# Kernel tuning notes

Measured on AMD Instinct MI355X. Metric: run time of the kernel, lower is better.

## Reference

```python
import jax, jax.numpy as jnp
import numpy as np

N_HEAD, D_MODEL, D_K, D_V = 16, 1024, 64, 64
B, S = 2, 2048
NEG = -1e10
LN_EPS = 1e-5

def setup_inputs() -> dict:
    key = jax.random.key(0)
    ks = jax.random.split(key, 10)
    std = 1.0 / np.sqrt(D_MODEL)
    return {
        "q": jax.random.normal(ks[0], (B, S, D_MODEL), jnp.float32),
        "k": jax.random.normal(ks[1], (B, S, D_MODEL), jnp.float32),
        "v": jax.random.normal(ks[2], (B, S, D_MODEL), jnp.float32),
        "mask": jnp.ones((B, 1, 1, S), jnp.int32),
        "Wq": jax.random.normal(ks[3], (D_MODEL, N_HEAD * D_K), jnp.float32) * std,
        "Wk": jax.random.normal(ks[4], (D_MODEL, N_HEAD * D_K), jnp.float32) * std,
        "Wv": jax.random.normal(ks[5], (D_MODEL, N_HEAD * D_V), jnp.float32) * std,
        "Wo": jax.random.normal(ks[6], (N_HEAD * D_V, D_MODEL), jnp.float32) * std,
        "bo": jnp.zeros((D_MODEL,), jnp.float32),
        "gamma": jnp.ones((D_MODEL,), jnp.float32),
        "beta": jnp.zeros((D_MODEL,), jnp.float32),
    }

def reference(q, k, v, mask, Wq, Wk, Wv, Wo, bo, gamma, beta):
    b, s, _ = q.shape
    scale = np.sqrt(D_MODEL)  # NOTE: original scales by sqrt(d_model), not sqrt(d_k)
    # project and split heads: [B,S,H,Dk] -> [B,H,S,Dk]
    qs = (q @ Wq).reshape(b, s, N_HEAD, D_K).transpose(0, 2, 1, 3)
    kk = (k @ Wk).reshape(b, -1, N_HEAD, D_K).transpose(0, 2, 1, 3)
    vs = (v @ Wv).reshape(b, -1, N_HEAD, D_V).transpose(0, 2, 1, 3)
    attn = jnp.einsum("bhqd,bhkd->bhqk", qs, kk) / scale
    attn = jnp.where(mask == 0, NEG, attn)
    attn = jax.nn.softmax(attn, axis=-1)  # dropout is identity in eval mode
    out = jnp.einsum("bhqk,bhkd->bhqd", attn, vs)
    out = out.transpose(0, 2, 1, 3).reshape(b, s, N_HEAD * D_V)
    out = out @ Wo + bo
    x = out + q
    mu = jnp.mean(x, axis=-1, keepdims=True)
    var = jnp.var(x, axis=-1, keepdims=True)
    out = (x - mu) * jax.lax.rsqrt(var + LN_EPS) * gamma + beta
    return out, attn
```

## Files before the change

kernel.cpp:

```cpp
#include <hip/hip_runtime.h>
#include <stdint.h>
#include <stddef.h>

#define NHEAD 16
#define DMODEL 1024
#define SS 2048
#define BB 2

typedef __attribute__((ext_vector_type(8))) short bf16x8;
typedef __attribute__((ext_vector_type(4))) float f32x4;
typedef __attribute__((ext_vector_type(4))) float floatv4;
typedef __attribute__((ext_vector_type(4))) unsigned short ushortv4;
typedef __attribute__((ext_vector_type(8))) unsigned short ushortv8;

#define MFMA16(A, B, C) __builtin_amdgcn_mfma_f32_16x16x32_bf16(A, B, C, 0, 0, 0)

__device__ __forceinline__ unsigned short f2bf(float f) {
    union { float f; unsigned u; } x;
    x.f = f;
    unsigned r = x.u + 0x7FFFu + ((x.u >> 16) & 1u);
    return (unsigned short)(r >> 16);
}

__device__ __forceinline__ unsigned short f2bf_trunc(float f) {
    union { float f; unsigned u; } x;
    x.f = f;
    return (unsigned short)(x.u >> 16);
}

__device__ __forceinline__ float bf2f(unsigned short u) {
    union { unsigned u; float f; } x;
    x.u = ((unsigned)u) << 16;
    return x.f;
}

__global__ __launch_bounds__(256) void cvt3(const float* __restrict__ q,
                                            const float* __restrict__ k,
                                            const float* __restrict__ v,
                                            unsigned short* __restrict__ qb,
                                            unsigned short* __restrict__ kb,
                                            unsigned short* __restrict__ vb, int n4) {
    int i = blockIdx.x * 256 + threadIdx.x;
    if (i >= n4) return;
    const float* src = blockIdx.y == 0 ? q : (blockIdx.y == 1 ? k : v);
    unsigned short* dst = blockIdx.y == 0 ? qb : (blockIdx.y == 1 ? kb : vb);
    floatv4 x = ((const floatv4*)src)[i];
    ushortv4 o;
    o.x = f2bf(x.x); o.y = f2bf(x.y); o.z = f2bf(x.z); o.w = f2bf(x.w);
    ((ushortv4*)dst)[i] = o;
}

__global__ __launch_bounds__(256) void wtrans4(
    const float* __restrict__ W0, const float* __restrict__ W1,
    const float* __restrict__ W2, const float* __restrict__ W3,
    unsigned short* __restrict__ T0, unsigned short* __restrict__ T1,
    unsigned short* __restrict__ T2, unsigned short* __restrict__ T3) {
    int sel = blockIdx.z;
    const float* W = sel == 0 ? W0 : (sel == 1 ? W1 : (sel == 2 ? W2 : W3));
    unsigned short* Wt = sel == 0 ? T0 : (sel == 1 ? T1 : (sel == 2 ? T2 : T3));
    float scl = (sel == 0) ? 0.03125f : 1.0f;
    __shared__ float tile[32][33];
    int tx = threadIdx.x & 31, ty = threadIdx.x >> 5;
    int nb = blockIdx.x * 32, kb = blockIdx.y * 32;
#pragma unroll
    for (int i = 0; i < 4; i++)
        tile[ty + i * 8][tx] = W[(size_t)(kb + ty + i * 8) * DMODEL + nb + tx];
    __syncthreads();
#pragma unroll
    for (int i = 0; i < 4; i++)
        Wt[(size_t)(nb + ty + i * 8) * DMODEL + kb + tx] = f2bf(tile[tx][ty + i * 8] * scl);
}

__device__ __forceinline__ void stage_tile_sw(const unsigned short* __restrict__ src, int ld,
                                              unsigned short* lds) {
    int t = threadIdx.x;
#pragma unroll
    for (int i = 0; i < 4; i++) {
        int pos = i * 256 + t;
        int row = pos >> 3;
        int g = pos & 7;
        int kcol = (g ^ (row & 7)) * 8;
        __builtin_amdgcn_global_load_lds(
            (__attribute__((address_space(1))) void*)(src + row * ld + kcol),
            (__attribute__((address_space(3))) void*)(lds + pos * 8), 16, 0, 0);
    }
}

__device__ __forceinline__ bf16x8 frag_ld(const unsigned short* lds, int row, int koff) {
    int idx = row * 64 + (koff ^ ((row & 7) << 3));
    return *(const bf16x8*)(lds + idx);
}

__device__ __forceinline__ void gemm_core(const unsigned short* __restrict__ A,
                                          const unsigned short* __restrict__ Bt,
                                          int mbase, int nbase,
                                          unsigned short* As, unsigned short* Bs,
                                          f32x4 acc[4][4]) {
    int tid = threadIdx.x;
    int w = tid >> 6, lane = tid & 63, lg = lane >> 4, li = lane & 15;
    int wm = w >> 1, wn = w & 1;
#pragma unroll
    for (int mi = 0; mi < 4; mi++)
#pragma unroll
        for (int ni = 0; ni < 4; ni++) acc[mi][ni] = f32x4{0.f, 0.f, 0.f, 0.f};

    for (int ks = 0; ks < DMODEL / 64; ks++) {
        __syncthreads();
        stage_tile_sw(A + (size_t)mbase * DMODEL + ks * 64, DMODEL, As);
        stage_tile_sw(Bt + (size_t)nbase * DMODEL + ks * 64, DMODEL, Bs);
        __syncthreads();
        bf16x8 af[2][4], bfr[2][4];
#pragma unroll
        for (int kc = 0; kc < 2; kc++) {
#pragma unroll
            for (int mi = 0; mi < 4; mi++)
                af[kc][mi] = frag_ld(As, wm * 64 + mi * 16 + li, kc * 32 + lg * 8);
#pragma unroll
            for (int ni = 0; ni < 4; ni++)
                bfr[kc][ni] = frag_ld(Bs, wn * 64 + ni * 16 + li, kc * 32 + lg * 8);
        }
#pragma unroll
        for (int kc = 0; kc < 2; kc++)
#pragma unroll
            for (int mi = 0; mi < 4; mi++)
#pragma unroll
                for (int ni = 0; ni < 4; ni++)
                    acc[mi][ni] = MFMA16(af[kc][mi], bfr[kc][ni], acc[mi][ni]);
    }
}

#define CS_STRIDE 136

__global__ __launch_bounds__(256) void gemm_qkv(
    const unsigned short* __restrict__ qb, const unsigned short* __restrict__ kbuf,
    const unsigned short* __restrict__ vb,
    const unsigned short* __restrict__ Wqt, const unsigned short* __restrict__ Wkt,
    const unsigned short* __restrict__ Wvt,
    unsigned short* __restrict__ Qp, unsigned short* __restrict__ Kp,
    unsigned short* __restrict__ Vt) {
    __shared__ unsigned short LDSbuf[128 * CS_STRIDE];
    unsigned short* As = LDSbuf;
    unsigned short* Bs = LDSbuf + 128 * 64;
    unsigned short* Cs = LDSbuf;

    int bid = blockIdx.y * 24 + blockIdx.x;
    int nl = (bid & 7) * 96 + (bid >> 3);
    int nt = nl % 24;
    int mbase = (nl / 24) * 128;
    int seg = nt >> 3;
    int nbase = (nt & 7) * 128;
    const unsigned short* A = seg == 0 ? qb : (seg == 1 ? kbuf : vb);
    const unsigned short* Bt = seg == 0 ? Wqt : (seg == 1 ? Wkt : Wvt);

    f32x4 acc[4][4];
    gemm_core(A, Bt, mbase, nbase, As, Bs, acc);

    int tid = threadIdx.x, w = tid >> 6, lane = tid & 63, lg = lane >> 4, li = lane & 15;
    int wm = w >> 1, wn = w & 1;

    __syncthreads();
    if (seg == 2) {
#pragma unroll
        for (int mi = 0; mi < 4; mi++)
#pragma unroll
            for (int ni = 0; ni < 4; ni++) {
                int nloc = wn * 64 + ni * 16 + li;
                int mloc = wm * 64 + mi * 16 + lg * 4;
#pragma unroll
                for (int r = 0; r < 4; r++)
                    Cs[nloc * CS_STRIDE + mloc + r] = f2bf(acc[mi][ni][r]);
            }
        __syncthreads();
#pragma unroll
        for (int i = 0; i < 8; i++) {
            int g = i * 256 + tid;
            int nloc = g >> 4, mo = (g & 15) * 8;
            int ng = nbase + nloc, h = ng >> 6, d = ng & 63;
            int m0 = mbase + mo, b = m0 >> 11, s0 = m0 & 2047;
            *(ushortv8*)(Vt + (((size_t)((b * NHEAD + h) * 64 + d)) << 11) + s0) =
                *(const ushortv8*)(Cs + nloc * CS_STRIDE + mo);
        }
    } else {
        unsigned short* Out = seg == 0 ? Qp : Kp;
#pragma unroll
        for (int mi = 0; mi < 4; mi++)
#pragma unroll
            for (int ni = 0; ni < 4; ni++) {
                int nloc = wn * 64 + ni * 16 + li;
                int mloc = wm * 64 + mi * 16 + lg * 4;
#pragma unroll
                for (int r = 0; r < 4; r++)
                    Cs[(mloc + r) * CS_STRIDE + nloc] = f2bf(acc[mi][ni][r]);
            }
        __syncthreads();
#pragma unroll
        for (int i = 0; i < 8; i++) {
            int g = i * 256 + tid;
            int row = g >> 4, on = (g & 15) * 8;
            int ng = nbase + on, h = ng >> 6, d = ng & 63;
            int m0 = mbase + row, b = m0 >> 11, s0 = m0 & 2047;
            *(ushortv8*)(Out + ((size_t)((b * NHEAD + h) * SS + s0)) * 64 + d) =
                *(const ushortv8*)(Cs + row * CS_STRIDE + on);
        }
    }
}

__global__ __launch_bounds__(256) void gemm_out(
    const unsigned short* __restrict__ Ob, const unsigned short* __restrict__ Wot,
    unsigned short* __restrict__ Yb) {
    __shared__ unsigned short LDSbuf[128 * CS_STRIDE];
    unsigned short* As = LDSbuf;
    unsigned short* Bs = LDSbuf + 128 * 64;
    unsigned short* Cs = LDSbuf;

    int bid = blockIdx.y * 8 + blockIdx.x;
    int nl = (bid & 7) * 32 + (bid >> 3);
    int nbase = (nl % 8) * 128;
    int mbase = (nl / 8) * 128;

    f32x4 acc[4][4];
    gemm_core(Ob, Wot, mbase, nbase, As, Bs, acc);

    int tid = threadIdx.x, w = tid >> 6, lane = tid & 63, lg = lane >> 4, li = lane & 15;
    int wm = w >> 1, wn = w & 1;

    __syncthreads();
#pragma unroll
    for (int mi = 0; mi < 4; mi++)
#pragma unroll
        for (int ni = 0; ni < 4; ni++) {
            int nloc = wn * 64 + ni * 16 + li;
            int mloc = wm * 64 + mi * 16 + lg * 4;
#pragma unroll
            for (int r = 0; r < 4; r++)
                Cs[(mloc + r) * CS_STRIDE + nloc] = f2bf(acc[mi][ni][r]);
        }
    __syncthreads();
#pragma unroll
    for (int i = 0; i < 8; i++) {
        int g = i * 256 + tid;
        int row = g >> 4, on = (g & 15) * 8;
        *(ushortv8*)(Yb + (size_t)(mbase + row) * DMODEL + nbase + on) =
            *(const ushortv8*)(Cs + row * CS_STRIDE + on);
    }
}

__device__ __forceinline__ void stage_kv(const unsigned short* __restrict__ Kb,
                                         const unsigned short* __restrict__ Vtb, int s0,
                                         unsigned short* kl, unsigned short* vl, int tid) {
#pragma unroll
    for (int i = 0; i < 2; i++) {
        int pos = i * 256 + tid;
        int row = pos >> 3, g = pos & 7;
        int col = (g ^ (row & 7)) * 8;
        __builtin_amdgcn_global_load_lds(
            (__attribute__((address_space(1))) void*)(Kb + (size_t)(s0 + row) * 64 + col),
            (__attribute__((address_space(3))) void*)(kl + pos * 8), 16, 0, 0);
    }
#pragma unroll
    for (int i = 0; i < 2; i++) {
        int pos = i * 256 + tid;
        int row = pos >> 3, g = pos & 7;
        int col = (g ^ (row & 7)) * 8;
        __builtin_amdgcn_global_load_lds(
            (__attribute__((address_space(1))) void*)(Vtb + (size_t)row * SS + s0 + col),
            (__attribute__((address_space(3))) void*)(vl + pos * 8), 16, 0, 0);
    }
}

__global__ __launch_bounds__(256, 2) void attn_fused(
    const unsigned short* __restrict__ Qp, const unsigned short* __restrict__ Kp,
    const unsigned short* __restrict__ Vt, const int* __restrict__ mask,
    float* __restrict__ attn_out, unsigned short* __restrict__ Ob) {
    __shared__ unsigned short Ks[2][64 * 64];
    __shared__ unsigned short Vs[2][64 * 64];
    __shared__ unsigned short Pl[4][32 * 64];
    __shared__ float Ml[SS];

    int blk = blockIdx.x;
    int xslot = blk & 7, rest = blk >> 3;
    int qt = rest & 15, bg = rest >> 4;
    int bh = bg * 8 + xslot, b = bh >> 4;
    int q0 = qt * 128;
    int tid = threadIdx.x, w = tid >> 6, lane = tid & 63, lg = lane >> 4, li = lane & 15;
    const unsigned short* Qb = Qp + (size_t)bh * SS * 64;
    const unsigned short* Kb = Kp + (size_t)bh * SS * 64;
    const unsigned short* Vtb = Vt + (size_t)bh * 64 * SS;
    const int* mb = mask + b * SS;
    int qw = q0 + w * 32;
    int sw = (li & 7) << 3;

    stage_kv(Kb, Vtb, 0, &Ks[0][0], &Vs[0][0], tid);

#pragma unroll
    for (int i = 0; i < SS / 256; i++) {
        int idx = i * 256 + tid;
        Ml[idx] = mb[idx] ? 0.f : -1e10f;
    }

    bf16x8 qa[2][2];
#pragma unroll
    for (int fq = 0; fq < 2; fq++) {
        int q = qw + fq * 16 + li;
        qa[fq][0] = *(const bf16x8*)(Qb + (size_t)q * 64 + lg * 8);
        qa[fq][1] = *(const bf16x8*)(Qb + (size_t)q * 64 + 32 + lg * 8);
    }

    f32x4 oacc[2][4];
#pragma unroll
    for (int fq = 0; fq < 2; fq++)
#pragma unroll
        for (int gd = 0; gd < 4; gd++) oacc[fq][gd] = f32x4{0.f, 0.f, 0.f, 0.f};
    float lsA[2] = {0.f, 0.f}, lsB[2] = {0.f, 0.f};
    unsigned short* Pw = &Pl[w][0];

    asm volatile("s_waitcnt vmcnt(0) lgkmcnt(0)" ::: "memory");
    __builtin_amdgcn_s_barrier();

#pragma unroll 1
    for (int t = 0; t < 32; t++) {
        int k0 = t * 64;
        if (t + 1 < 32)
            stage_kv(Kb, Vtb, k0 + 64, &Ks[(t + 1) & 1][0], &Vs[(t + 1) & 1][0], tid);
        __builtin_amdgcn_sched_barrier(0);
        const unsigned short* Kc = &Ks[t & 1][0];
        const unsigned short* Vc = &Vs[t & 1][0];
#pragma unroll
        for (int fk = 0; fk < 4; fk++) {
            int row = fk * 16 + li;
            bf16x8 kf0 = *(const bf16x8*)(Kc + row * 64 + ((lg * 8) ^ sw));
            bf16x8 kf1 = *(const bf16x8*)(Kc + row * 64 + ((32 + lg * 8) ^ sw));
            floatv4 mk = *(const floatv4*)(Ml + k0 + fk * 16 + lg * 4);
#pragma unroll
            for (int fq = 0; fq < 2; fq++) {
                f32x4 sc = f32x4{0.f, 0.f, 0.f, 0.f};
                sc = MFMA16(kf0, qa[fq][0], sc);
                sc = MFMA16(kf1, qa[fq][1], sc);
                floatv4 pv;
#pragma unroll
                for (int r = 0; r < 4; r++)
                    pv[r] = __expf(fminf(sc[r] + mk[r], 80.f));
                lsA[fq] += pv[0] + pv[1];
                lsB[fq] += pv[2] + pv[3];
                ushortv4 pk;
#pragma unroll
                for (int r = 0; r < 4; r++) pk[r] = f2bf_trunc(pv[r]);
                *(ushortv4*)(Pw + (fq * 16 + li) * 64 + ((fk * 16 + lg * 4) ^ sw)) = pk;
            }
        }
#pragma unroll
        for (int kc = 0; kc < 2; kc++) {
            bf16x8 vf[4];
#pragma unroll
            for (int gd = 0; gd < 4; gd++) {
                int vrow = gd * 16 + li;
                vf[gd] = *(const bf16x8*)(Vc + vrow * 64 + ((kc * 32 + lg * 8) ^ sw));
            }
#pragma unroll
            for (int fq = 0; fq < 2; fq++) {
                bf16x8 pa = *(const bf16x8*)(Pw + (fq * 16 + li) * 64 +
                                             ((kc * 32 + lg * 8) ^ sw));
#pragma unroll
                for (int gd = 0; gd < 4; gd++)
                    oacc[fq][gd] = MFMA16(pa, vf[gd], oacc[fq][gd]);
            }
        }
        asm volatile("s_waitcnt vmcnt(0)" ::: "memory");
        __builtin_amdgcn_s_barrier();
    }

    float linvv[2];
    float* LinvW = (float*)Pw;
#pragma unroll
    for (int fq = 0; fq < 2; fq++) {
        float lsum = lsA[fq] + lsB[fq];
        lsum += __shfl_xor(lsum, 16);
        lsum += __shfl_xor(lsum, 32);
        linvv[fq] = 1.0f / lsum;
        if (lg == 0) LinvW[fq * 16 + li] = linvv[fq];
    }
    int h = bh & 15;
#pragma unroll
    for (int fq = 0; fq < 2; fq++)
#pragma unroll
        for (int gd = 0; gd < 4; gd++)
#pragma unroll
            for (int r = 0; r < 4; r++) {
                int srow = qw + fq * 16 + lg * 4 + r;
                float o = oacc[fq][gd][r] * LinvW[fq * 16 + lg * 4 + r];
                Ob[(size_t)(b * SS + srow) * DMODEL + h * 64 + gd * 16 + li] = f2bf(o);
            }

    float* ar0 = attn_out + ((size_t)bh * SS + qw + li) * SS + lg * 4;
    float* ar1 = ar0 + (size_t)16 * SS;
#pragma unroll 1
    for (int kt = 0; kt < 16; kt++) {
        int k0 = kt * 128;
#pragma unroll
        for (int fk = 0; fk < 8; fk++) {
            const unsigned short* kp = Kb + (size_t)(k0 + fk * 16 + li) * 64;
            bf16x8 kf0 = *(const bf16x8*)(kp + lg * 8);
            bf16x8 kf1 = *(const bf16x8*)(kp + 32 + lg * 8);
            floatv4 mk = *(const floatv4*)(Ml + k0 + fk * 16 + lg * 4);
#pragma unroll
            for (int fq = 0; fq < 2; fq++) {
                f32x4 sc = f32x4{0.f, 0.f, 0.f, 0.f};
                sc = MFMA16(kf0, qa[fq][0], sc);
                sc = MFMA16(kf1, qa[fq][1], sc);
                floatv4 pv;
#pragma unroll
                for (int r = 0; r < 4; r++)
                    pv[r] = __expf(fminf(sc[r] + mk[r], 80.f)) * linvv[fq];
                *(floatv4*)((fq == 0 ? ar0 : ar1) + k0 + fk * 16) = pv;
            }
        }
    }
}

__global__ __launch_bounds__(256) void ln_kernel(const unsigned short* __restrict__ Yb,
                                                 const float* __restrict__ qres,
                                                 const float* __restrict__ bo,
                                                 const float* __restrict__ gamma,
                                                 const float* __restrict__ beta,
                                                 float* __restrict__ out) {
    int row = blockIdx.x;
    int t = threadIdx.x;
    ushortv4 yv = ((const ushortv4*)(Yb + (size_t)row * DMODEL))[t];
    floatv4 qv = ((const floatv4*)(qres + (size_t)row * DMODEL))[t];
    floatv4 bv = ((const floatv4*)bo)[t];
    floatv4 v;
    v.x = bf2f(yv.x) + bv.x + qv.x;
    v.y = bf2f(yv.y) + bv.y + qv.y;
    v.z = bf2f(yv.z) + bv.z + qv.z;
    v.w = bf2f(yv.w) + bv.w + qv.w;
    float s1 = v.x + v.y + v.z + v.w;
    float s2 = v.x * v.x + v.y * v.y + v.z * v.z + v.w * v.w;
#pragma unroll
    for (int m = 1; m < 64; m <<= 1) { s1 += __shfl_xor(s1, m); s2 += __shfl_xor(s2, m); }
    __shared__ float red[8];
    int w = t >> 6, lane = t & 63;
    if (lane == 0) { red[w] = s1; red[4 + w] = s2; }
    __syncthreads();
    s1 = red[0] + red[1] + red[2] + red[3];
    s2 = red[4] + red[5] + red[6] + red[7];
    float mu = s1 * (1.0f / DMODEL);
    float var = s2 * (1.0f / DMODEL) - mu * mu;
    float rstd = rsqrtf(var + 1e-5f);
    floatv4 g = ((const floatv4*)gamma)[t];
    floatv4 bb = ((const floatv4*)beta)[t];
    floatv4 o;
    o.x = (v.x - mu) * rstd * g.x + bb.x;
    o.y = (v.y - mu) * rstd * g.y + bb.y;
    o.z = (v.z - mu) * rstd * g.z + bb.z;
    o.w = (v.w - mu) * rstd * g.w + bb.w;
    ((floatv4*)(out + (size_t)row * DMODEL))[t] = o;
}

extern "C" void kernel_launch(void* const* d_in, const int* in_sizes, int n_in,
                              void* d_out, int out_size, void* d_ws, size_t ws_size,
                              hipStream_t stream) {
    const float* q = (const float*)d_in[0];
    const float* k = (const float*)d_in[1];
    const float* v = (const float*)d_in[2];
    const int* mask = (const int*)d_in[3];
    const float* Wq = (const float*)d_in[4];
    const float* Wk = (const float*)d_in[5];
    const float* Wv = (const float*)d_in[6];
    const float* Wo = (const float*)d_in[7];
    const float* bo = (const float*)d_in[8];
    const float* gamma = (const float*)d_in[9];
    const float* beta = (const float*)d_in[10];

    float* out = (float*)d_out;
    float* attn = out + (size_t)BB * SS * DMODEL;

    const size_t NTOK = (size_t)BB * SS;
    unsigned short* qb = (unsigned short*)d_ws;
    unsigned short* kb = qb + NTOK * DMODEL;
    unsigned short* vb = kb + NTOK * DMODEL;
    unsigned short* Wqt = vb + NTOK * DMODEL;
    unsigned short* Wkt = Wqt + (size_t)DMODEL * DMODEL;
    unsigned short* Wvt = Wkt + (size_t)DMODEL * DMODEL;
    unsigned short* Wot = Wvt + (size_t)DMODEL * DMODEL;
    unsigned short* Qp = Wot + (size_t)DMODEL * DMODEL;
    unsigned short* Kp = Qp + NTOK * DMODEL;
    unsigned short* Vt = Kp + NTOK * DMODEL;
    unsigned short* Ob = Vt + NTOK * DMODEL;
    unsigned short* Yb = qb;

    const int n4 = (int)(NTOK * DMODEL / 4);
    cvt3<<<dim3(n4 / 256, 3), 256, 0, stream>>>(q, k, v, qb, kb, vb, n4);
    wtrans4<<<dim3(32, 32, 4), 256, 0, stream>>>(Wq, Wk, Wv, Wo, Wqt, Wkt, Wvt, Wot);

    gemm_qkv<<<dim3(24, 32), 256, 0, stream>>>(qb, kb, vb, Wqt, Wkt, Wvt, Qp, Kp, Vt);

    attn_fused<<<512, 256, 0, stream>>>(Qp, Kp, Vt, mask, attn, Ob);

    gemm_out<<<dim3(8, 32), 256, 0, stream>>>(Ob, Wot, Yb);

    ln_kernel<<<(int)NTOK, 256, 0, stream>>>(Yb, q, bo, gamma, beta, out);
}
```

Measured before the change: 301.5 us.

## Split fused attention into output kernel and separate attention-probability writer kernel

Splits the fused attention kernel in two. The first kernel computes the output and stores per-row inverse softmax sums to global memory. It keeps the mask in LDS as bf16 to shrink shared memory and raises the occupancy hint to 3 blocks per CU. A second kernel with 4x more blocks recomputes QK^T over key slices and writes the large fp32 attention matrix, spreading that write-bound phase across more parallel blocks. The cost is an extra launch and recomputing scores a second time.

```diff
diff --git a/kernel.cpp b/kernel.cpp
--- a/kernel.cpp
+++ b/kernel.cpp
@@ -268,14 +268,14 @@
     }
 }
 
-__global__ __launch_bounds__(256, 2) void attn_fused(
+__global__ __launch_bounds__(256, 3) void attn_o(
     const unsigned short* __restrict__ Qp, const unsigned short* __restrict__ Kp,
     const unsigned short* __restrict__ Vt, const int* __restrict__ mask,
-    float* __restrict__ attn_out, unsigned short* __restrict__ Ob) {
+    float* __restrict__ linvG, unsigned short* __restrict__ Ob) {
     __shared__ unsigned short Ks[2][64 * 64];
     __shared__ unsigned short Vs[2][64 * 64];
     __shared__ unsigned short Pl[4][32 * 64];
-    __shared__ float Ml[SS];
+    __shared__ unsigned short Mlb[SS];
 
     int blk = blockIdx.x;
     int xslot = blk & 7, rest = blk >> 3;
@@ -295,7 +295,7 @@
 #pragma unroll
     for (int i = 0; i < SS / 256; i++) {
         int idx = i * 256 + tid;
-        Ml[idx] = mb[idx] ? 0.f : -1e10f;
+        Mlb[idx] = mb[idx] ? (unsigned short)0 : f2bf_trunc(-1e10f);
     }
 
     bf16x8 qa[2][2];
@@ -330,7 +330,10 @@
             int row = fk * 16 + li;
             bf16x8 kf0 = *(const bf16x8*)(Kc + row * 64 + ((lg * 8) ^ sw));
             bf16x8 kf1 = *(const bf16x8*)(Kc + row * 64 + ((32 + lg * 8) ^ sw));
-            floatv4 mk = *(const floatv4*)(Ml + k0 + fk * 16 + lg * 4);
+            ushortv4 mku = *(const ushortv4*)(Mlb + k0 + fk * 16 + lg * 4);
+            float mkf[4];
+#pragma unroll
+            for (int r = 0; r < 4; r++) mkf[r] = bf2f(mku[r]);
 #pragma unroll
             for (int fq = 0; fq < 2; fq++) {
                 f32x4 sc = f32x4{0.f, 0.f, 0.f, 0.f};
@@ -339,7 +342,7 @@
                 floatv4 pv;
 #pragma unroll
                 for (int r = 0; r < 4; r++)
-                    pv[r] = __expf(fminf(sc[r] + mk[r], 80.f));
+                    pv[r] = __expf(fminf(sc[r] + mkf[r], 80.f));
                 lsA[fq] += pv[0] + pv[1];
                 lsB[fq] += pv[2] + pv[3];
                 ushortv4 pk;
@@ -377,7 +380,10 @@
         lsum += __shfl_xor(lsum, 16);
         lsum += __shfl_xor(lsum, 32);
         linvv[fq] = 1.0f / lsum;
-        if (lg == 0) LinvW[fq * 16 + li] = linvv[fq];
+        if (lg == 0) {
+            LinvW[fq * 16 + li] = linvv[fq];
+            linvG[(size_t)bh * SS + qw + fq * 16 + li] = linvv[fq];
+        }
     }
     int h = bh & 15;
 #pragma unroll
@@ -390,15 +396,52 @@
                 float o = oacc[fq][gd][r] * LinvW[fq * 16 + lg * 4 + r];
                 Ob[(size_t)(b * SS + srow) * DMODEL + h * 64 + gd * 16 + li] = f2bf(o);
             }
-
-    float* ar0 = attn_out + ((size_t)bh * SS + qw + li) * SS + lg * 4;
+}
+
+__global__ __launch_bounds__(256) void attn_p(
+    const unsigned short* __restrict__ Qp, const unsigned short* __restrict__ Kp,
+    const int* __restrict__ mask, const float* __restrict__ linvG,
+    float* __restrict__ attn_out) {
+    __shared__ float Ml[512];
+    int blk = blockIdx.x;
+    int xslot = blk & 7, rest = blk >> 3;
+    int qt = rest & 15; rest >>= 4;
+    int ksl = rest & 3; rest >>= 2;
+    int bg = rest;
+    int bh = bg * 8 + xslot, b = bh >> 4;
+    int q0 = qt * 128;
+    int kbase = ksl * 512;
+    int tid = threadIdx.x, w = tid >> 6, lane = tid & 63, lg = lane >> 4, li = lane & 15;
+    const unsigned short* Qb = Qp + (size_t)bh * SS * 64;
+    const unsigned short* Kb = Kp + (size_t)bh * SS * 64;
+    const int* mb = mask + b * SS + kbase;
+    int qw = q0 + w * 32;
+
+#pragma unroll
+    for (int i = 0; i < 2; i++) {
+        int idx = i * 256 + tid;
+        Ml[idx] = mb[idx] ? 0.f : -1e10f;
+    }
+    __syncthreads();
+
+    bf16x8 qa[2][2];
+    float lv[2];
+#pragma unroll
+    for (int fq = 0; fq < 2; fq++) {
+        int q = qw + fq * 16 + li;
+        qa[fq][0] = *(const bf16x8*)(Qb + (size_t)q * 64 + lg * 8);
+        qa[fq][1] = *(const bf16x8*)(Qb + (size_t)q * 64 + 32 + lg * 8);
+        lv[fq] = linvG[(size_t)bh * SS + q];
+    }
+    float* ar0 = attn_out + ((size_t)bh * SS + qw + li) * SS + kbase + lg * 4;
     float* ar1 = ar0 + (size_t)16 * SS;
+
 #pragma unroll 1
-    for (int kt = 0; kt < 16; kt++) {
+    for (int kt = 0; kt < 4; kt++) {
         int k0 = kt * 128;
 #pragma unroll
         for (int fk = 0; fk < 8; fk++) {
-            const unsigned short* kp = Kb + (size_t)(k0 + fk * 16 + li) * 64;
+            const unsigned short* kp = Kb + (size_t)(kbase + k0 + fk * 16 + li) * 64;
             bf16x8 kf0 = *(const bf16x8*)(kp + lg * 8);
             bf16x8 kf1 = *(const bf16x8*)(kp + 32 + lg * 8);
             floatv4 mk = *(const floatv4*)(Ml + k0 + fk * 16 + lg * 4);
@@ -410,7 +453,7 @@
                 floatv4 pv;
 #pragma unroll
                 for (int r = 0; r < 4; r++)
-                    pv[r] = __expf(fminf(sc[r] + mk[r], 80.f)) * linvv[fq];
+                    pv[r] = __expf(fminf(sc[r] + mk[r], 80.f)) * lv[fq];
                 *(floatv4*)((fq == 0 ? ar0 : ar1) + k0 + fk * 16) = pv;
             }
         }
@@ -486,6 +529,7 @@
     unsigned short* Kp = Qp + NTOK * DMODEL;
     unsigned short* Vt = Kp + NTOK * DMODEL;
     unsigned short* Ob = Vt + NTOK * DMODEL;
+    float* linvG = (float*)(Ob + NTOK * DMODEL);
     unsigned short* Yb = qb;
 
     const int n4 = (int)(NTOK * DMODEL / 4);
@@ -494,7 +538,8 @@
 
     gemm_qkv<<<dim3(24, 32), 256, 0, stream>>>(qb, kb, vb, Wqt, Wkt, Wvt, Qp, Kp, Vt);
 
-    attn_fused<<<512, 256, 0, stream>>>(Qp, Kp, Vt, mask, attn, Ob);
+    attn_o<<<512, 256, 0, stream>>>(Qp, Kp, Vt, mask, linvG, Ob);
+    attn_p<<<2048, 256, 0, stream>>>(Qp, Kp, mask, linvG, attn);
 
     gemm_out<<<dim3(8, 32), 256, 0, stream>>>(Ob, Wot, Yb);
 
```

Measured after the change: 349.9 us. 1.16x slower.

## Stage attention-probability writes through LDS for coalesced rows; merge prep kernels

Applied to the files above, without the earlier changes.

The attention-probability output pass now writes each 64-column tile into a per-wave swizzled LDS buffer, reusing the freed K/V/P shared memory, then reads it back so each row segment goes to global memory as contiguous 256-byte stores. Before, each lane wrote scattered 16-byte chunks across rows. This targets the large fp32 attn write, which dominates memory traffic. Separately, the bf16 conversion and weight-transpose kernels are merged into one launch to save a kernel launch. The cost is extra LDS traffic and a barrier.

```diff
diff --git a/kernel.cpp b/kernel.cpp
--- a/kernel.cpp
+++ b/kernel.cpp
@@ -34,41 +34,43 @@
     return x.f;
 }
 
-__global__ __launch_bounds__(256) void cvt3(const float* __restrict__ q,
-                                            const float* __restrict__ k,
-                                            const float* __restrict__ v,
-                                            unsigned short* __restrict__ qb,
-                                            unsigned short* __restrict__ kb,
-                                            unsigned short* __restrict__ vb, int n4) {
-    int i = blockIdx.x * 256 + threadIdx.x;
-    if (i >= n4) return;
-    const float* src = blockIdx.y == 0 ? q : (blockIdx.y == 1 ? k : v);
-    unsigned short* dst = blockIdx.y == 0 ? qb : (blockIdx.y == 1 ? kb : vb);
-    floatv4 x = ((const floatv4*)src)[i];
-    ushortv4 o;
-    o.x = f2bf(x.x); o.y = f2bf(x.y); o.z = f2bf(x.z); o.w = f2bf(x.w);
-    ((ushortv4*)dst)[i] = o;
-}
-
-__global__ __launch_bounds__(256) void wtrans4(
+__global__ __launch_bounds__(256) void prep(
+    const float* __restrict__ q, const float* __restrict__ k, const float* __restrict__ v,
+    unsigned short* __restrict__ qb, unsigned short* __restrict__ kb,
+    unsigned short* __restrict__ vb,
     const float* __restrict__ W0, const float* __restrict__ W1,
     const float* __restrict__ W2, const float* __restrict__ W3,
     unsigned short* __restrict__ T0, unsigned short* __restrict__ T1,
     unsigned short* __restrict__ T2, unsigned short* __restrict__ T3) {
-    int sel = blockIdx.z;
-    const float* W = sel == 0 ? W0 : (sel == 1 ? W1 : (sel == 2 ? W2 : W3));
-    unsigned short* Wt = sel == 0 ? T0 : (sel == 1 ? T1 : (sel == 2 ? T2 : T3));
-    float scl = (sel == 0) ? 0.03125f : 1.0f;
     __shared__ float tile[32][33];
-    int tx = threadIdx.x & 31, ty = threadIdx.x >> 5;
-    int nb = blockIdx.x * 32, kb = blockIdx.y * 32;
-#pragma unroll
-    for (int i = 0; i < 4; i++)
-        tile[ty + i * 8][tx] = W[(size_t)(kb + ty + i * 8) * DMODEL + nb + tx];
-    __syncthreads();
-#pragma unroll
-    for (int i = 0; i < 4; i++)
-        Wt[(size_t)(nb + ty + i * 8) * DMODEL + kb + tx] = f2bf(tile[tx][ty + i * 8] * scl);
+    int blk = blockIdx.x;
+    if (blk < 12288) {
+        int which = blk >> 12;
+        int i = (blk & 4095) * 256 + threadIdx.x;
+        const float* src = which == 0 ? q : (which == 1 ? k : v);
+        unsigned short* dst = which == 0 ? qb : (which == 1 ? kb : vb);
+        floatv4 x = ((const floatv4*)src)[i];
+        ushortv4 o;
+        o.x = f2bf(x.x); o.y = f2bf(x.y); o.z = f2bf(x.z); o.w = f2bf(x.w);
+        ((ushortv4*)dst)[i] = o;
+    } else {
+        int t = blk - 12288;
+        int sel = t >> 10;
+        int rest = t & 1023;
+        const float* W = sel == 0 ? W0 : (sel == 1 ? W1 : (sel == 2 ? W2 : W3));
+        unsigned short* Wt = sel == 0 ? T0 : (sel == 1 ? T1 : (sel == 2 ? T2 : T3));
+        float scl = (sel == 0) ? 0.03125f : 1.0f;
+        int tx = threadIdx.x & 31, ty = threadIdx.x >> 5;
+        int nb = (rest & 31) * 32, kb2 = (rest >> 5) * 32;
+#pragma unroll
+        for (int i = 0; i < 4; i++)
+            tile[ty + i * 8][tx] = W[(size_t)(kb2 + ty + i * 8) * DMODEL + nb + tx];
+        __syncthreads();
+#pragma unroll
+        for (int i = 0; i < 4; i++)
+            Wt[(size_t)(nb + ty + i * 8) * DMODEL + kb2 + tx] =
+                f2bf(tile[tx][ty + i * 8] * scl);
+    }
 }
 
 __device__ __forceinline__ void stage_tile_sw(const unsigned short* __restrict__ src, int ld,
@@ -272,10 +274,11 @@
     const unsigned short* __restrict__ Qp, const unsigned short* __restrict__ Kp,
     const unsigned short* __restrict__ Vt, const int* __restrict__ mask,
     float* __restrict__ attn_out, unsigned short* __restrict__ Ob) {
-    __shared__ unsigned short Ks[2][64 * 64];
-    __shared__ unsigned short Vs[2][64 * 64];
-    __shared__ unsigned short Pl[4][32 * 64];
-    __shared__ float Ml[SS];
+    __shared__ __align__(16) unsigned short SH[28672];
+    unsigned short* KsB = SH;
+    unsigned short* VsB = SH + 8192;
+    unsigned short* PlB = SH + 16384;
+    float* Ml = (float*)(SH + 24576);
 
     int blk = blockIdx.x;
     int xslot = blk & 7, rest = blk >> 3;
@@ -290,7 +293,7 @@
     int qw = q0 + w * 32;
     int sw = (li & 7) << 3;
 
-    stage_kv(Kb, Vtb, 0, &Ks[0][0], &Vs[0][0], tid);
+    stage_kv(Kb, Vtb, 0, KsB, VsB, tid);
 
 #pragma unroll
     for (int i = 0; i < SS / 256; i++) {
@@ -312,7 +315,7 @@
 #pragma unroll
         for (int gd = 0; gd < 4; gd++) oacc[fq][gd] = f32x4{0.f, 0.f, 0.f, 0.f};
     float lsA[2] = {0.f, 0.f}, lsB[2] = {0.f, 0.f};
-    unsigned short* Pw = &Pl[w][0];
+    unsigned short* Pw = PlB + w * (32 * 64);
 
     asm volatile("s_waitcnt vmcnt(0) lgkmcnt(0)" ::: "memory");
     __builtin_amdgcn_s_barrier();
@@ -321,10 +324,11 @@
     for (int t = 0; t < 32; t++) {
         int k0 = t * 64;
         if (t + 1 < 32)
-            stage_kv(Kb, Vtb, k0 + 64, &Ks[(t + 1) & 1][0], &Vs[(t + 1) & 1][0], tid);
+            stage_kv(Kb, Vtb, k0 + 64, KsB + ((t + 1) & 1) * 4096,
+                     VsB + ((t + 1) & 1) * 4096, tid);
         __builtin_amdgcn_sched_barrier(0);
-        const unsigned short* Kc = &Ks[t & 1][0];
-        const unsigned short* Vc = &Vs[t & 1][0];
+        const unsigned short* Kc = KsB + (t & 1) * 4096;
+        const unsigned short* Vc = VsB + (t & 1) * 4096;
 #pragma unroll
         for (int fk = 0; fk < 4; fk++) {
             int row = fk * 16 + li;
@@ -391,13 +395,15 @@
                 Ob[(size_t)(b * SS + srow) * DMODEL + h * 64 + gd * 16 + li] = f2bf(o);
             }
 
-    float* ar0 = attn_out + ((size_t)bh * SS + qw + li) * SS + lg * 4;
-    float* ar1 = ar0 + (size_t)16 * SS;
+    __builtin_amdgcn_s_barrier();
+    float* Pt = (float*)SH + w * 2048;
+    int rgrp = lane >> 4;
+
 #pragma unroll 1
-    for (int kt = 0; kt < 16; kt++) {
-        int k0 = kt * 128;
-#pragma unroll
-        for (int fk = 0; fk < 8; fk++) {
+    for (int t = 0; t < 32; t++) {
+        int k0 = t * 64;
+#pragma unroll
+        for (int fk = 0; fk < 4; fk++) {
             const unsigned short* kp = Kb + (size_t)(k0 + fk * 16 + li) * 64;
             bf16x8 kf0 = *(const bf16x8*)(kp + lg * 8);
             bf16x8 kf1 = *(const bf16x8*)(kp + 32 + lg * 8);
@@ -411,8 +417,16 @@
 #pragma unroll
                 for (int r = 0; r < 4; r++)
                     pv[r] = __expf(fminf(sc[r] + mk[r], 80.f)) * linvv[fq];
-                *(floatv4*)((fq == 0 ? ar0 : ar1) + k0 + fk * 16) = pv;
-            }
+                int prow = fq * 16 + li;
+                *(floatv4*)(Pt + prow * 64 + ((fk * 16 + lg * 4) ^ ((prow & 7) << 3))) = pv;
+            }
+        }
+#pragma unroll
+        for (int g = 0; g < 8; g++) {
+            int row = g * 4 + rgrp;
+            int colb = li * 4;
+            floatv4 vv = *(const floatv4*)(Pt + row * 64 + (colb ^ ((row & 7) << 3)));
+            *(floatv4*)(attn_out + ((size_t)bh * SS + qw + row) * SS + k0 + colb) = vv;
         }
     }
 }
@@ -488,9 +502,8 @@
     unsigned short* Ob = Vt + NTOK * DMODEL;
     unsigned short* Yb = qb;
 
-    const int n4 = (int)(NTOK * DMODEL / 4);
-    cvt3<<<dim3(n4 / 256, 3), 256, 0, stream>>>(q, k, v, qb, kb, vb, n4);
-    wtrans4<<<dim3(32, 32, 4), 256, 0, stream>>>(Wq, Wk, Wv, Wo, Wqt, Wkt, Wvt, Wot);
+    prep<<<16384, 256, 0, stream>>>(q, k, v, qb, kb, vb, Wq, Wk, Wv, Wo,
+                                    Wqt, Wkt, Wvt, Wot);
 
     gemm_qkv<<<dim3(24, 32), 256, 0, stream>>>(qb, kb, vb, Wqt, Wkt, Wvt, Qp, Kp, Vt);
 
```

Measured after the change: 277.1 us. 1.09x faster.
